# Optimization experiments

Measured on AMD Instinct MI355X. Metric: run time of the kernel, lower is better.

## Reference

```python
import jax, jax.numpy as jnp
import numpy as np

INF = 1e9
EPS = 1e-5

def layer_norm(x, g, b):
    mu = jnp.mean(x, axis=-1, keepdims=True)
    var = jnp.mean(jnp.square(x - mu), axis=-1, keepdims=True)
    return (x - mu) * jax.lax.rsqrt(var + EPS) * g + b

def setup_inputs() -> dict:
    key = jax.random.key(0)
    ks = jax.random.split(key, 12)
    B, S, N = 1, 512, 384
    c_in, c_hid, c_z, H = 64, 32, 128, 8
    d = c_hid * H
    sc = lambda fan: 1.0 / np.sqrt(fan)
    return {
        "m": jax.random.normal(ks[0], (B, S, N, c_in), jnp.float32),
        "z": jax.random.normal(ks[1], (B, N, N, c_z), jnp.float32),
        "mask": jnp.ones((B, N, N), jnp.float32),
        "gamma_m": jnp.ones((c_in,), jnp.float32),
        "beta_m": jnp.zeros((c_in,), jnp.float32),
        "gamma_z": jnp.ones((c_z,), jnp.float32),
        "beta_z": jnp.zeros((c_z,), jnp.float32),
        "w_z": jax.random.normal(ks[2], (c_z, H), jnp.float32) * sc(c_z),
        "b_z": jnp.zeros((H,), jnp.float32),
        "w_v": jax.random.normal(ks[3], (c_in, d), jnp.float32) * sc(c_in),
        "b_v": jnp.zeros((d,), jnp.float32),
        "w_g": jax.random.normal(ks[4], (c_in, d), jnp.float32) * sc(c_in),
        "b_g": jnp.zeros((d,), jnp.float32),
        "w_o": jax.random.normal(ks[5], (d, c_in), jnp.float32) * sc(d),
        "b_o": jnp.zeros((c_in,), jnp.float32),
    }

def reference(m, z, mask, gamma_m, beta_m, gamma_z, beta_z,
              w_z, b_z, w_v, b_v, w_g, b_g, w_o, b_o):
    B, S, N, c_in = m.shape
    H = w_z.shape[-1]
    C = w_v.shape[-1] // H
    # pair branch: LN -> linear -> [B,H,Nq,Nk] logits + mask bias -> softmax
    zn = layer_norm(z, gamma_z, beta_z)
    logits = jnp.einsum('bqkz,zh->bhqk', zn, w_z) + b_z[None, :, None, None]
    logits = logits + (INF * (mask - 1.0))[:, None, :, :]
    w = jax.nn.softmax(logits, axis=-1)                      # [B,H,Nq,Nk]
    # MSA branch: LN -> value / gate projections
    mn = layer_norm(m, gamma_m, beta_m)
    v = (mn @ w_v + b_v).reshape(B, S, N, H, C)              # [B,S,Nk,H,C]
    o = jnp.einsum('bhqk,bskhc->bsqhc', w, v)                # broadcast over S
    g = jax.nn.sigmoid(mn @ w_g + b_g).reshape(B, S, N, H, C)
    out = (o * g).reshape(B, S, N, H * C) @ w_o + b_o
    return out
```

## Files before the change

### kernel.cpp

```cpp
#include <hip/hip_runtime.h>
#include <hip/hip_bf16.h>

#define INFV 1e9f
#define EPSV 1e-5f

typedef unsigned short u16;
typedef unsigned int u32;
typedef __attribute__((ext_vector_type(8))) short short8;
typedef __attribute__((ext_vector_type(4))) float float4v;

__device__ __forceinline__ u16 f2us(float f) {
    u32 v;
    __builtin_memcpy(&v, &f, 4);
    u32 r = v + 0x7fffu + ((v >> 16) & 1u);
    return (u16)(r >> 16);
}

__device__ __forceinline__ float wred_sum(float x) {
    #pragma unroll
    for (int o = 32; o; o >>= 1) x += __shfl_xor(x, o);
    return x;
}
__device__ __forceinline__ float wred_max(float x) {
    #pragma unroll
    for (int o = 32; o; o >>= 1) x = fmaxf(x, __shfl_xor(x, o));
    return x;
}

__device__ __forceinline__ void gld16(const void* g, void* l) {
    __builtin_amdgcn_global_load_lds(
        (const __attribute__((address_space(1))) unsigned int*)g,
        (__attribute__((address_space(3))) unsigned int*)l,
        16, 0, 0);
}

__global__ __launch_bounds__(256) void k_prep_ln(
    const float* __restrict__ m, const float* __restrict__ gm, const float* __restrict__ bm,
    u16* __restrict__ mn,
    const float* __restrict__ wv, const float* __restrict__ wg,
    const float* __restrict__ wo, const float* __restrict__ wz,
    u16* __restrict__ wv_t, u16* __restrict__ wg_t,
    u16* __restrict__ wo_t, u16* __restrict__ wzT)
{
    if (blockIdx.x < 12288) {
        const int tid  = threadIdx.x;
        const int wid  = tid >> 6;
        const int lane = tid & 63;
        const int rloc = lane >> 4;
        const int c4   = (lane & 15) * 4;
        const int row  = blockIdx.x * 16 + wid * 4 + rloc;
        const float4 x = *(const float4*)(m + (size_t)row * 64 + c4);
        float s1 = x.x + x.y + x.z + x.w;
        float s2 = x.x * x.x + x.y * x.y + x.z * x.z + x.w * x.w;
        #pragma unroll
        for (int o = 8; o; o >>= 1) { s1 += __shfl_xor(s1, o); s2 += __shfl_xor(s2, o); }
        const float mean = s1 * (1.0f / 64.0f);
        const float var  = s2 * (1.0f / 64.0f) - mean * mean;
        const float rs   = rsqrtf(var + EPSV);
        const float4 g = *(const float4*)(gm + c4);
        const float4 b = *(const float4*)(bm + c4);
        uint2 pk;
        pk.x = (u32)f2us((x.x - mean) * rs * g.x + b.x) | ((u32)f2us((x.y - mean) * rs * g.y + b.y) << 16);
        pk.y = (u32)f2us((x.z - mean) * rs * g.z + b.z) | ((u32)f2us((x.w - mean) * rs * g.w + b.w) << 16);
        *(uint2*)(mn + (size_t)row * 64 + c4) = pk;
    } else {
        const int i = (blockIdx.x - 12288) * 256 + threadIdx.x;
        if (i < 16384) {
            const int n = i >> 6, k = i & 63;
            wv_t[i] = f2us(wv[(size_t)k * 256 + n]);
        } else if (i < 32768) {
            const int j = i - 16384, n = j >> 6, k = j & 63;
            wg_t[j] = f2us(wg[(size_t)k * 256 + n]);
        } else if (i < 49152) {
            const int j = i - 32768, n = j >> 8, k = j & 255;
            wo_t[j] = f2us(wo[(size_t)k * 64 + n]);
        } else if (i < 51200) {
            const int j = i - 49152, n = j >> 7, k = j & 127;
            wzT[j] = (n < 8) ? f2us(wz[(size_t)k * 8 + n]) : (u16)0;
        }
    }
}

__global__ __launch_bounds__(256) void k_vT(
    const u16* __restrict__ mn, const u16* __restrict__ wv_t, u16* __restrict__ vTf)
{
    const int tid  = threadIdx.x;
    const int wid  = tid >> 6;
    const int lane = tid & 63;
    const int lrow = lane & 15;
    const int lkg  = lane >> 4;
    const int s    = blockIdx.y;
    const int k0   = blockIdx.x * 64 + wid * 16;

    const int kt   = blockIdx.x * 2 + (wid >> 1);
    const int lkgc = (wid & 1) * 2 + (lkg >> 1);
    const int joff = (lkg & 1) * 4;

    const u16* mnk = mn + ((size_t)s * 384 + k0 + lrow) * 64;
    const short8 a0 = *(const short8*)(mnk + lkg * 8);
    const short8 a1 = *(const short8*)(mnk + 32 + lkg * 8);

    #pragma unroll
    for (int nt = 0; nt < 16; nt++) {
        const short8 b0 = *(const short8*)(wv_t + (size_t)(nt * 16 + lrow) * 64 + lkg * 8);
        const short8 b1 = *(const short8*)(wv_t + (size_t)(nt * 16 + lrow) * 64 + 32 + lkg * 8);
        float4v acc = (float4v){0.f, 0.f, 0.f, 0.f};
        acc = __builtin_amdgcn_mfma_f32_16x16x32_bf16(a0, b0, acc, 0, 0, 0);
        acc = __builtin_amdgcn_mfma_f32_16x16x32_bf16(a1, b1, acc, 0, 0, 0);
        uint2 pk;
        pk.x = (u32)f2us(acc[0]) | ((u32)f2us(acc[1]) << 16);
        pk.y = (u32)f2us(acc[2]) | ((u32)f2us(acc[3]) << 16);
        *(uint2*)(vTf + ((((size_t)s * 12 + kt) * 16 + nt) << 9)
                      + ((lkgc << 4) + lrow) * 8 + joff) = pk;
    }
}

__global__ __launch_bounds__(256) void k_logits2(
    const float* __restrict__ z, const float* __restrict__ mask,
    const float* __restrict__ gz, const float* __restrict__ bz,
    const u16* __restrict__ wzT, const float* __restrict__ bzb,
    float* __restrict__ wbuf)
{
    const int tid   = threadIdx.x;
    const int wid   = tid >> 6;
    const int lane  = tid & 63;
    const int lrow  = lane & 15;
    const int lkg   = lane >> 4;
    const int pair0 = (blockIdx.x * 4 + wid) * 16;

    float x[4][8];
    float s1 = 0.0f, s2 = 0.0f;
    #pragma unroll
    for (int ks = 0; ks < 4; ks++) {
        const float4* zp = (const float4*)(z + (size_t)(pair0 + lrow) * 128 + ks * 32 + lkg * 8);
        const float4 a = zp[0], b = zp[1];
        x[ks][0] = a.x; x[ks][1] = a.y; x[ks][2] = a.z; x[ks][3] = a.w;
        x[ks][4] = b.x; x[ks][5] = b.y; x[ks][6] = b.z; x[ks][7] = b.w;
        #pragma unroll
        for (int j = 0; j < 8; j++) { s1 += x[ks][j]; s2 += x[ks][j] * x[ks][j]; }
    }
    s1 += __shfl_xor(s1, 16); s1 += __shfl_xor(s1, 32);
    s2 += __shfl_xor(s2, 16); s2 += __shfl_xor(s2, 32);
    const float mean = s1 * (1.0f / 128.0f);
    const float var  = s2 * (1.0f / 128.0f) - mean * mean;
    const float rs   = rsqrtf(var + EPSV);

    float4v acc = (float4v){0.f, 0.f, 0.f, 0.f};
    #pragma unroll
    for (int ks = 0; ks < 4; ks++) {
        const int c0 = ks * 32 + lkg * 8;
        const float4 g0 = *(const float4*)(gz + c0);
        const float4 g1 = *(const float4*)(gz + c0 + 4);
        const float4 b0 = *(const float4*)(bz + c0);
        const float4 b1 = *(const float4*)(bz + c0 + 4);
        const float gv[8] = {g0.x, g0.y, g0.z, g0.w, g1.x, g1.y, g1.z, g1.w};
        const float bvv[8] = {b0.x, b0.y, b0.z, b0.w, b1.x, b1.y, b1.z, b1.w};
        short8 afr;
        #pragma unroll
        for (int j = 0; j < 8; j++)
            afr[j] = (short)f2us((x[ks][j] - mean) * rs * gv[j] + bvv[j]);
        const short8 bfr = *(const short8*)(wzT + (size_t)lrow * 128 + c0);
        acc = __builtin_amdgcn_mfma_f32_16x16x32_bf16(afr, bfr, acc, 0, 0, 0);
    }
    if (lrow < 8) {
        const float bzv = bzb[lrow];
        #pragma unroll
        for (int r = 0; r < 4; r++) {
            const int p = pair0 + lkg * 4 + r;
            const float mb = INFV * (mask[p] - 1.0f);
            wbuf[(size_t)lrow * 147456 + p] = acc[r] + bzv + mb;
        }
    }
}

__global__ __launch_bounds__(256) void k_softmax_f2(
    const float* __restrict__ wbuf, u16* __restrict__ wbf)
{
    __shared__ __align__(16) u16 lds[16 * 392];

    const int tid  = threadIdx.x;
    const int w    = tid >> 6;
    const int lane = tid & 63;
    const int rg   = lane >> 4;
    const int l16  = lane & 15;

    const int bx = blockIdx.x;
    const int h  = bx & 7;
    const int qm = bx >> 3;
    const int qb = qm >> 1;
    const int mt = qm & 1;
    const int rb = w * 4 + rg;
    const int q  = qb * 32 + mt * 16 + rb;

    const float* base = wbuf + (size_t)h * 147456 + (size_t)q * 384 + l16 * 24;
    float v[24];
    float mx = -1e30f;
    #pragma unroll
    for (int i = 0; i < 6; i++) {
        const float4 x = *(const float4*)(base + i * 4);
        v[i * 4 + 0] = x.x; v[i * 4 + 1] = x.y; v[i * 4 + 2] = x.z; v[i * 4 + 3] = x.w;
        mx = fmaxf(mx, fmaxf(fmaxf(x.x, x.y), fmaxf(x.z, x.w)));
    }
    #pragma unroll
    for (int o = 8; o; o >>= 1) mx = fmaxf(mx, __shfl_xor(mx, o));
    float s = 0.0f;
    #pragma unroll
    for (int i = 0; i < 24; i++) { v[i] = __expf(v[i] - mx); s += v[i]; }
    #pragma unroll
    for (int o = 8; o; o >>= 1) s += __shfl_xor(s, o);
    const float inv = 1.0f / s;

    u16* lp = lds + rb * 392 + l16 * 24;
    #pragma unroll
    for (int i = 0; i < 12; i++) {
        const u32 pk = (u32)f2us(v[2 * i] * inv) | ((u32)f2us(v[2 * i + 1] * inv) << 16);
        *(u32*)(lp + 2 * i) = pk;
    }
    __syncthreads();

    const int lr  = lane & 15;
    const int lkg = lane >> 4;
    #pragma unroll
    for (int j = 0; j < 3; j++) {
        const int kt = w * 3 + j;
        const short8 f = *(const short8*)(lds + lr * 392 + kt * 32 + lkg * 8);
        *(short8*)(wbf + ((((size_t)(qb * 8 + h) * 12 + kt) * 2 + mt) << 9) + lane * 8) = f;
    }
}

__global__ __launch_bounds__(256) void k_softmax(
    const float* __restrict__ wbuf, u16* __restrict__ wb16)
{
    const int r = blockIdx.x * 4 + (threadIdx.x >> 6);
    const int lane = threadIdx.x & 63;
    const float* base = wbuf + (size_t)r * 384;
    float v[6];
    float mx = -1e30f;
    #pragma unroll
    for (int j = 0; j < 6; j++) {
        v[j] = base[lane + j * 64];
        mx = fmaxf(mx, v[j]);
    }
    mx = wred_max(mx);
    float s = 0.0f;
    #pragma unroll
    for (int j = 0; j < 6; j++) {
        v[j] = __expf(v[j] - mx);
        s += v[j];
    }
    s = wred_sum(s);
    const float inv = 1.0f / s;
    u16* ob = wb16 + (size_t)r * 384;
    #pragma unroll
    for (int j = 0; j < 6; j++) ob[lane + j * 64] = f2us(v[j] * inv);
}

__global__ __launch_bounds__(512, 4) void k_fused9(
    const u16* __restrict__ mn, const u16* __restrict__ vTf,
    const float* __restrict__ bv, const float* __restrict__ bg, const float* __restrict__ bo,
    const u16* __restrict__ wg_t, const u16* __restrict__ wo_t,
    const u16* __restrict__ wbf, float* __restrict__ out)
{
    __shared__ __align__(16) char smem[67584];
    u16* vtt = (u16*)smem;
    u16* og  = (u16*)smem;

    const int tid  = threadIdx.x;
    const int w    = tid >> 6;
    const int wq   = w >> 1;
    const int wh   = w & 1;
    const int lane = tid & 63;
    const int lrow = lane & 15;
    const int lkg  = lane >> 4;
    const int stg  = w * 4;

    const int bid  = blockIdx.x;
    const int xcd  = bid & 7;
    const int slot = bid >> 3;
    const int sdiv = slot / 3;
    const int q0   = (slot - sdiv * 3) * 128;
    const int s    = sdiv * 8 + xcd;

    const int qb = (q0 >> 5) + wq;

    float4v oacc[16];
    #pragma unroll
    for (int mt = 0; mt < 2; mt++)
        #pragma unroll
        for (int nt = 0; nt < 8; nt++) {
            const float b = bv[wh * 128 + nt * 16 + lrow];
            oacc[mt * 8 + nt] = (float4v){b, b, b, b};
        }

    const u16* vfs = vTf + (((size_t)s * 12) << 13);

    {
        const u16* gp = vfs + ((size_t)stg << 9) + lane * 8;
        u16* lp = vtt + stg * 512;
        #pragma unroll
        for (int i = 0; i < 4; i++) gld16(gp + i * 512, lp + i * 512);
    }
    __syncthreads();

    for (int pt = 0; pt < 6; pt++) {
        const int cur = pt & 1;
        if (pt < 5) {
            const u16* gp = vfs + ((size_t)((pt + 1) * 32 + stg) << 9) + lane * 8;
            u16* lp = vtt + ((cur ^ 1) * 32 + stg) * 512;
            #pragma unroll
            for (int i = 0; i < 4; i++) gld16(gp + i * 512, lp + i * 512);
        }
        #pragma unroll 1
        for (int sub = 0; sub < 2; sub++) {
            const int kt = pt * 2 + sub;
            const u16* vb = vtt + (cur * 32 + sub * 16) * 512;
            #pragma unroll
            for (int hl = 0; hl < 4; hl++) {
                const size_t abase = (((size_t)(qb * 8 + wh * 4 + hl) * 12 + kt) * 2) << 9;
                const short8 a0 = *(const short8*)(wbf + abase + lane * 8);
                const short8 a1 = *(const short8*)(wbf + abase + 512 + lane * 8);
                const short8 b0 = *(const short8*)(vb + ((wh * 8 + hl * 2) * 512) + lane * 8);
                const short8 b1 = *(const short8*)(vb + ((wh * 8 + hl * 2 + 1) * 512) + lane * 8);
                const int nt = hl * 2;
                oacc[nt]         = __builtin_amdgcn_mfma_f32_16x16x32_bf16(a0, b0, oacc[nt], 0, 0, 0);
                oacc[8 + nt]     = __builtin_amdgcn_mfma_f32_16x16x32_bf16(a1, b0, oacc[8 + nt], 0, 0, 0);
                oacc[nt + 1]     = __builtin_amdgcn_mfma_f32_16x16x32_bf16(a0, b1, oacc[nt + 1], 0, 0, 0);
                oacc[8 + nt + 1] = __builtin_amdgcn_mfma_f32_16x16x32_bf16(a1, b1, oacc[8 + nt + 1], 0, 0, 0);
            }
        }
        __syncthreads();
    }

    {
        const u16* mnq = mn + ((size_t)s * 384 + q0 + wq * 32 + lrow) * 64;
        #pragma unroll
        for (int mt = 0; mt < 2; mt++) {
            const short8 a0 = *(const short8*)(mnq + mt * 1024 + lkg * 8);
            const short8 a1 = *(const short8*)(mnq + mt * 1024 + 32 + lkg * 8);
            #pragma unroll
            for (int nt = 0; nt < 8; nt++) {
                const int hc0 = wh * 128 + nt * 16;
                const float bgv = bg[hc0 + lrow];
                const short8 b0 = *(const short8*)(wg_t + (size_t)(hc0 + lrow) * 64 + lkg * 8);
                const short8 b1 = *(const short8*)(wg_t + (size_t)(hc0 + lrow) * 64 + 32 + lkg * 8);
                float4v gacc = (float4v){bgv, bgv, bgv, bgv};
                gacc = __builtin_amdgcn_mfma_f32_16x16x32_bf16(a0, b0, gacc, 0, 0, 0);
                gacc = __builtin_amdgcn_mfma_f32_16x16x32_bf16(a1, b1, gacc, 0, 0, 0);
                #pragma unroll
                for (int r = 0; r < 4; r++) {
                    const float sg = 1.0f / (1.0f + __expf(-gacc[r]));
                    og[(size_t)(wq * 32 + mt * 16 + lkg * 4 + r) * 264 + hc0 + lrow]
                        = f2us(oacc[mt * 8 + nt][r] * sg);
                }
            }
        }
    }
    __syncthreads();

    #pragma unroll
    for (int mt = 0; mt < 2; mt++) {
        short8 af[8];
        #pragma unroll
        for (int ks = 0; ks < 8; ks++)
            af[ks] = *(const short8*)&og[(size_t)(wq * 32 + mt * 16 + lrow) * 264 + ks * 32 + lkg * 8];
        #pragma unroll
        for (int ntl = 0; ntl < 2; ntl++) {
            const int nto = wh * 2 + ntl;
            const float bov = bo[nto * 16 + lrow];
            float4v fac = (float4v){bov, bov, bov, bov};
            #pragma unroll
            for (int ks = 0; ks < 8; ks++) {
                const short8 b = *(const short8*)(wo_t + (size_t)(nto * 16 + lrow) * 256 + ks * 32 + lkg * 8);
                fac = __builtin_amdgcn_mfma_f32_16x16x32_bf16(af[ks], b, fac, 0, 0, 0);
            }
            #pragma unroll
            for (int r = 0; r < 4; r++)
                out[((size_t)s * 384 + q0 + wq * 32 + mt * 16 + lkg * 4 + r) * 64 + nto * 16 + lrow]
                    = fac[r];
        }
    }
}

__global__ __launch_bounds__(256, 2) void k_fused4(
    const u16* __restrict__ mn,
    const float* __restrict__ bv, const float* __restrict__ bg, const float* __restrict__ bo,
    const u16* __restrict__ wv_t, const u16* __restrict__ wg_t, const u16* __restrict__ wo_t,
    const u16* __restrict__ wb16, float* __restrict__ out)
{
    __shared__ __align__(16) char smem[67584];
    u16* vtt = (u16*)smem;
    u16* og  = (u16*)smem;

    const int tid  = threadIdx.x;
    const int wid  = tid >> 6;
    const int lane = tid & 63;
    const int lrow = lane & 15;
    const int lkg  = lane >> 4;
    const int s    = blockIdx.y;
    const int q0   = blockIdx.x * 128;

    const int vmt  = wid & 1;
    const int vnt0 = (wid >> 1) * 8;

    float4v oacc[32];
    #pragma unroll
    for (int mt = 0; mt < 2; mt++)
        #pragma unroll
        for (int nt = 0; nt < 16; nt++) {
            const float b = bv[nt * 16 + lrow];
            oacc[mt * 16 + nt] = (float4v){b, b, b, b};
        }

    for (int kt = 0; kt < 12; kt++) {
        const int k0 = kt * 32;
        float4v vacc[8];
        #pragma unroll
        for (int nt = 0; nt < 8; nt++) vacc[nt] = (float4v){0.f, 0.f, 0.f, 0.f};
        const u16* mnk = mn + ((size_t)s * 384 + k0 + vmt * 16 + lrow) * 64;
        #pragma unroll
        for (int ks = 0; ks < 2; ks++) {
            const short8 a = *(const short8*)(mnk + ks * 32 + lkg * 8);
            #pragma unroll
            for (int nt = 0; nt < 8; nt++) {
                const short8 b = *(const short8*)(wv_t + (size_t)((vnt0 + nt) * 16 + lrow) * 64 + ks * 32 + lkg * 8);
                vacc[nt] = __builtin_amdgcn_mfma_f32_16x16x32_bf16(a, b, vacc[nt], 0, 0, 0);
            }
        }
        u16* vb = vtt + (size_t)(kt & 1) * 8192;
        const int kg8 = vmt * 2 + (lkg >> 1);
        const int ko  = (lkg & 1) * 4;
        #pragma unroll
        for (int nt = 0; nt < 8; nt++) {
            uint2 pk;
            pk.x = (u32)f2us(vacc[nt][0]) | ((u32)f2us(vacc[nt][1]) << 16);
            pk.y = (u32)f2us(vacc[nt][2]) | ((u32)f2us(vacc[nt][3]) << 16);
            *(uint2*)&vb[((size_t)kg8 * 256 + (vnt0 + nt) * 16 + lrow) * 8 + ko] = pk;
        }
        __syncthreads();

        short8 ah[2][8];
        #pragma unroll
        for (int mt = 0; mt < 2; mt++)
            #pragma unroll
            for (int h = 0; h < 8; h++)
                ah[mt][h] = *(const short8*)(wb16 + (size_t)h * 147456
                              + (size_t)(q0 + wid * 32 + mt * 16 + lrow) * 384 + k0 + lkg * 8);
        #pragma unroll
        for (int nt = 0; nt < 16; nt++) {
            const short8 b = *(const short8*)&vb[((size_t)lkg * 256 + nt * 16 + lrow) * 8];
            oacc[nt]      = __builtin_amdgcn_mfma_f32_16x16x32_bf16(ah[0][nt >> 1], b, oacc[nt], 0, 0, 0);
            oacc[16 + nt] = __builtin_amdgcn_mfma_f32_16x16x32_bf16(ah[1][nt >> 1], b, oacc[16 + nt], 0, 0, 0);
        }
    }
    __syncthreads();

    #pragma unroll
    for (int mt = 0; mt < 2; mt++) {
        const u16* mnq = mn + ((size_t)s * 384 + q0 + wid * 32 + mt * 16 + lrow) * 64;
        const short8 a0 = *(const short8*)(mnq + lkg * 8);
        const short8 a1 = *(const short8*)(mnq + 32 + lkg * 8);
        #pragma unroll
        for (int nt = 0; nt < 16; nt++) {
            const float bgv = bg[nt * 16 + lrow];
            float4v gacc = (float4v){bgv, bgv, bgv, bgv};
            const short8 b0 = *(const short8*)(wg_t + (size_t)(nt * 16 + lrow) * 64 + lkg * 8);
            const short8 b1 = *(const short8*)(wg_t + (size_t)(nt * 16 + lrow) * 64 + 32 + lkg * 8);
            gacc = __builtin_amdgcn_mfma_f32_16x16x32_bf16(a0, b0, gacc, 0, 0, 0);
            gacc = __builtin_amdgcn_mfma_f32_16x16x32_bf16(a1, b1, gacc, 0, 0, 0);
            #pragma unroll
            for (int r = 0; r < 4; r++) {
                const float sg = 1.0f / (1.0f + __expf(-gacc[r]));
                og[(size_t)(wid * 32 + mt * 16 + lkg * 4 + r) * 264 + nt * 16 + lrow]
                    = f2us(oacc[mt * 16 + nt][r] * sg);
            }
        }
    }
    __syncthreads();

    #pragma unroll
    for (int mt = 0; mt < 2; mt++) {
        short8 af[8];
        #pragma unroll
        for (int ks = 0; ks < 8; ks++)
            af[ks] = *(const short8*)&og[(size_t)(wid * 32 + mt * 16 + lrow) * 264 + ks * 32 + lkg * 8];
        #pragma unroll
        for (int nt = 0; nt < 4; nt++) {
            const float bov = bo[nt * 16 + lrow];
            float4v fac = (float4v){bov, bov, bov, bov};
            #pragma unroll
            for (int ks = 0; ks < 8; ks++) {
                const short8 b = *(const short8*)(wo_t + (size_t)(nt * 16 + lrow) * 256 + ks * 32 + lkg * 8);
                fac = __builtin_amdgcn_mfma_f32_16x16x32_bf16(af[ks], b, fac, 0, 0, 0);
            }
            #pragma unroll
            for (int r = 0; r < 4; r++)
                out[((size_t)s * 384 + q0 + wid * 32 + mt * 16 + lkg * 4 + r) * 64 + nt * 16 + lrow]
                    = fac[r];
        }
    }
}

extern "C" void kernel_launch(void* const* d_in, const int* in_sizes, int n_in,
                              void* d_out, int out_size, void* d_ws, size_t ws_size,
                              hipStream_t stream) {
    const float* m    = (const float*)d_in[0];
    const float* z    = (const float*)d_in[1];
    const float* mask = (const float*)d_in[2];
    const float* gm   = (const float*)d_in[3];
    const float* bm   = (const float*)d_in[4];
    const float* gz   = (const float*)d_in[5];
    const float* bz   = (const float*)d_in[6];
    const float* wz   = (const float*)d_in[7];
    const float* bzb  = (const float*)d_in[8];
    const float* wv   = (const float*)d_in[9];
    const float* bv   = (const float*)d_in[10];
    const float* wg   = (const float*)d_in[11];
    const float* bg   = (const float*)d_in[12];
    const float* wo   = (const float*)d_in[13];
    const float* bo   = (const float*)d_in[14];
    float* out = (float*)d_out;

    char* ws = (char*)d_ws;
    float* wbuf = (float*)ws;
    u16*  wb16  = (u16*)(ws + 4718592);
    u16*  mn    = (u16*)(ws + 7077888);
    u16*  wv_t  = (u16*)(ws + 32243712);
    u16*  wg_t  = (u16*)(ws + 32276480);
    u16*  wo_t  = (u16*)(ws + 32309248);
    u16*  wzT   = (u16*)(ws + 32342016);
    u16*  vTf   = (u16*)(ws + 32346112);

    const bool big = ws_size >= 133009408ull;

    k_prep_ln<<<12488, 256, 0, stream>>>(m, gm, bm, mn, wv, wg, wo, wz, wv_t, wg_t, wo_t, wzT);
    if (big)
        k_vT<<<dim3(6, 512), 256, 0, stream>>>(mn, wv_t, vTf);
    k_logits2<<<2304, 256, 0, stream>>>(z, mask, gz, bz, wzT, bzb, wbuf);
    if (big) {
        k_softmax_f2<<<192, 256, 0, stream>>>(wbuf, wb16);
        k_fused9<<<1536, 512, 0, stream>>>(mn, vTf, bv, bg, bo, wg_t, wo_t, wb16, out);
    } else {
        k_softmax<<<768, 256, 0, stream>>>(wbuf, wb16);
        k_fused4<<<dim3(3, 512), 256, 0, stream>>>(mn, bv, bg, bo, wv_t, wg_t, wo_t, wb16, out);
    }
}
```

Measured before the change: 386.9 us.

## Process two MSA rows per block to reuse attention weight fragments

The fused attention/gate/output kernel now runs 1024-thread blocks that each cover two sequence rows (s0, s0+1) for a 128-query tile. Each wave loads its softmax-weight A fragments once per k-tile and applies them to the V tiles of both rows, which halves global reads of the weight matrix. The wave-to-head split is re-partitioned so each wave owns 4 head-column tiles, and LDS doubles to about 132KB. The larger LDS footprint and block size cut occupancy to one block per CU, which may limit latency hiding.

```diff
diff --git a/kernel.cpp b/kernel.cpp
--- a/kernel.cpp
+++ b/kernel.cpp
@@ -255,91 +255,97 @@
     for (int j = 0; j < 6; j++) ob[lane + j * 64] = f2us(v[j] * inv);
 }
 
-__global__ __launch_bounds__(512, 4) void k_fused9(
+__global__ __launch_bounds__(1024, 4) void k_fused11(
     const u16* __restrict__ mn, const u16* __restrict__ vTf,
     const float* __restrict__ bv, const float* __restrict__ bg, const float* __restrict__ bo,
     const u16* __restrict__ wg_t, const u16* __restrict__ wo_t,
     const u16* __restrict__ wbf, float* __restrict__ out)
 {
-    __shared__ __align__(16) char smem[67584];
+    __shared__ __align__(16) char smem[135168];
     u16* vtt = (u16*)smem;
     u16* og  = (u16*)smem;
 
     const int tid  = threadIdx.x;
     const int w    = tid >> 6;
-    const int wq   = w >> 1;
-    const int wh   = w & 1;
+    const int wq   = w & 3;
+    const int wh   = (w >> 2) & 3;
     const int lane = tid & 63;
     const int lrow = lane & 15;
     const int lkg  = lane >> 4;
-    const int stg  = w * 4;
 
     const int bid  = blockIdx.x;
     const int xcd  = bid & 7;
     const int slot = bid >> 3;
-    const int sdiv = slot / 3;
-    const int q0   = (slot - sdiv * 3) * 128;
-    const int s    = sdiv * 8 + xcd;
+    const int spd  = slot / 3;
+    const int qi   = slot - spd * 3;
+    const int q0   = qi * 128;
+    const int sp   = spd * 8 + xcd;
+    const int s0   = sp * 2;
 
     const int qb = (q0 >> 5) + wq;
 
     float4v oacc[16];
     #pragma unroll
-    for (int mt = 0; mt < 2; mt++)
-        #pragma unroll
-        for (int nt = 0; nt < 8; nt++) {
-            const float b = bv[wh * 128 + nt * 16 + lrow];
-            oacc[mt * 8 + nt] = (float4v){b, b, b, b};
-        }
-
-    const u16* vfs = vTf + (((size_t)s * 12) << 13);
+    for (int ntl = 0; ntl < 4; ntl++) {
+        const float b = bv[(wh * 4 + ntl) * 16 + lrow];
+        #pragma unroll
+        for (int sm = 0; sm < 4; sm++) oacc[sm * 4 + ntl] = (float4v){b, b, b, b};
+    }
+
+    const u16* wAb0 = wbf + (((size_t)(qb * 8 + wh * 2 + 0) * 24) << 9);
+    const u16* wAb1 = wbf + (((size_t)(qb * 8 + wh * 2 + 1) * 24) << 9);
+
+    const int ssg  = (w * 2) >> 4;
+    const int nt0  = (w * 2) & 15;
+    const u16* vstg = vTf + ((((size_t)(s0 + ssg) * 12) * 16 + nt0) << 9) + lane * 8;
 
     {
-        const u16* gp = vfs + ((size_t)stg << 9) + lane * 8;
-        u16* lp = vtt + stg * 512;
-        #pragma unroll
-        for (int i = 0; i < 4; i++) gld16(gp + i * 512, lp + i * 512);
+        u16* lp = vtt + (ssg * 16 + nt0) * 512;
+        gld16(vstg, lp);
+        gld16(vstg + 512, lp + 512);
     }
     __syncthreads();
 
-    for (int pt = 0; pt < 6; pt++) {
-        const int cur = pt & 1;
-        if (pt < 5) {
-            const u16* gp = vfs + ((size_t)((pt + 1) * 32 + stg) << 9) + lane * 8;
-            u16* lp = vtt + ((cur ^ 1) * 32 + stg) * 512;
-            #pragma unroll
-            for (int i = 0; i < 4; i++) gld16(gp + i * 512, lp + i * 512);
-        }
-        #pragma unroll 1
-        for (int sub = 0; sub < 2; sub++) {
-            const int kt = pt * 2 + sub;
-            const u16* vb = vtt + (cur * 32 + sub * 16) * 512;
-            #pragma unroll
-            for (int hl = 0; hl < 4; hl++) {
-                const size_t abase = (((size_t)(qb * 8 + wh * 4 + hl) * 12 + kt) * 2) << 9;
-                const short8 a0 = *(const short8*)(wbf + abase + lane * 8);
-                const short8 a1 = *(const short8*)(wbf + abase + 512 + lane * 8);
-                const short8 b0 = *(const short8*)(vb + ((wh * 8 + hl * 2) * 512) + lane * 8);
-                const short8 b1 = *(const short8*)(vb + ((wh * 8 + hl * 2 + 1) * 512) + lane * 8);
-                const int nt = hl * 2;
-                oacc[nt]         = __builtin_amdgcn_mfma_f32_16x16x32_bf16(a0, b0, oacc[nt], 0, 0, 0);
-                oacc[8 + nt]     = __builtin_amdgcn_mfma_f32_16x16x32_bf16(a1, b0, oacc[8 + nt], 0, 0, 0);
-                oacc[nt + 1]     = __builtin_amdgcn_mfma_f32_16x16x32_bf16(a0, b1, oacc[nt + 1], 0, 0, 0);
-                oacc[8 + nt + 1] = __builtin_amdgcn_mfma_f32_16x16x32_bf16(a1, b1, oacc[8 + nt + 1], 0, 0, 0);
+    for (int kt = 0; kt < 12; kt++) {
+        const int cur = kt & 1;
+        if (kt < 11) {
+            const u16* gp = vstg + (((size_t)(kt + 1) * 16) << 9);
+            u16* lp = vtt + (((cur ^ 1) * 2 + ssg) * 16 + nt0) * 512;
+            gld16(gp, lp);
+            gld16(gp + 512, lp + 512);
+        }
+        const size_t aoff = (size_t)kt << 10;
+        const short8 a00 = *(const short8*)(wAb0 + aoff + lane * 8);
+        const short8 a01 = *(const short8*)(wAb0 + aoff + 512 + lane * 8);
+        const short8 a10 = *(const short8*)(wAb1 + aoff + lane * 8);
+        const short8 a11 = *(const short8*)(wAb1 + aoff + 512 + lane * 8);
+        #pragma unroll
+        for (int ss = 0; ss < 2; ss++) {
+            const u16* vb = vtt + ((cur * 2 + ss) * 16 + wh * 4) * 512;
+            #pragma unroll
+            for (int ntl = 0; ntl < 4; ntl++) {
+                const short8 b = *(const short8*)(vb + ntl * 512 + lane * 8);
+                const short8 am0 = (ntl < 2) ? a00 : a10;
+                const short8 am1 = (ntl < 2) ? a01 : a11;
+                oacc[ss * 8 + ntl]     = __builtin_amdgcn_mfma_f32_16x16x32_bf16(am0, b, oacc[ss * 8 + ntl], 0, 0, 0);
+                oacc[ss * 8 + 4 + ntl] = __builtin_amdgcn_mfma_f32_16x16x32_bf16(am1, b, oacc[ss * 8 + 4 + ntl], 0, 0, 0);
             }
         }
         __syncthreads();
     }
 
-    {
+    #pragma unroll
+    for (int ss = 0; ss < 2; ss++) {
+        const int s = s0 + ss;
         const u16* mnq = mn + ((size_t)s * 384 + q0 + wq * 32 + lrow) * 64;
+        u16* ogs = og + ss * 33792;
         #pragma unroll
         for (int mt = 0; mt < 2; mt++) {
             const short8 a0 = *(const short8*)(mnq + mt * 1024 + lkg * 8);
             const short8 a1 = *(const short8*)(mnq + mt * 1024 + 32 + lkg * 8);
             #pragma unroll
-            for (int nt = 0; nt < 8; nt++) {
-                const int hc0 = wh * 128 + nt * 16;
+            for (int ntl = 0; ntl < 4; ntl++) {
+                const int hc0 = (wh * 4 + ntl) * 16;
                 const float bgv = bg[hc0 + lrow];
                 const short8 b0 = *(const short8*)(wg_t + (size_t)(hc0 + lrow) * 64 + lkg * 8);
                 const short8 b1 = *(const short8*)(wg_t + (size_t)(hc0 + lrow) * 64 + 32 + lkg * 8);
@@ -349,34 +355,42 @@
                 #pragma unroll
                 for (int r = 0; r < 4; r++) {
                     const float sg = 1.0f / (1.0f + __expf(-gacc[r]));
-                    og[(size_t)(wq * 32 + mt * 16 + lkg * 4 + r) * 264 + hc0 + lrow]
-                        = f2us(oacc[mt * 8 + nt][r] * sg);
+                    ogs[(size_t)(wq * 32 + mt * 16 + lkg * 4 + r) * 264 + hc0 + lrow]
+                        = f2us(oacc[ss * 8 + mt * 4 + ntl][r] * sg);
                 }
             }
         }
     }
     __syncthreads();
 
-    #pragma unroll
-    for (int mt = 0; mt < 2; mt++) {
-        short8 af[8];
-        #pragma unroll
-        for (int ks = 0; ks < 8; ks++)
-            af[ks] = *(const short8*)&og[(size_t)(wq * 32 + mt * 16 + lrow) * 264 + ks * 32 + lkg * 8];
-        #pragma unroll
-        for (int ntl = 0; ntl < 2; ntl++) {
-            const int nto = wh * 2 + ntl;
-            const float bov = bo[nto * 16 + lrow];
-            float4v fac = (float4v){bov, bov, bov, bov};
-            #pragma unroll
-            for (int ks = 0; ks < 8; ks++) {
-                const short8 b = *(const short8*)(wo_t + (size_t)(nto * 16 + lrow) * 256 + ks * 32 + lkg * 8);
-                fac = __builtin_amdgcn_mfma_f32_16x16x32_bf16(af[ks], b, fac, 0, 0, 0);
+    {
+        const int ws  = w >> 3;
+        const int w8  = w & 7;
+        const int wq8 = w8 >> 1;
+        const int wh8 = w8 & 1;
+        const int s   = s0 + ws;
+        const u16* ogs = og + ws * 33792;
+        #pragma unroll
+        for (int mt = 0; mt < 2; mt++) {
+            short8 af[8];
+            #pragma unroll
+            for (int ks = 0; ks < 8; ks++)
+                af[ks] = *(const short8*)(ogs + (size_t)(wq8 * 32 + mt * 16 + lrow) * 264 + ks * 32 + lkg * 8);
+            #pragma unroll
+            for (int ntl = 0; ntl < 2; ntl++) {
+                const int nto = wh8 * 2 + ntl;
+                const float bov = bo[nto * 16 + lrow];
+                float4v fac = (float4v){bov, bov, bov, bov};
+                #pragma unroll
+                for (int ks = 0; ks < 8; ks++) {
+                    const short8 b = *(const short8*)(wo_t + (size_t)(nto * 16 + lrow) * 256 + ks * 32 + lkg * 8);
+                    fac = __builtin_amdgcn_mfma_f32_16x16x32_bf16(af[ks], b, fac, 0, 0, 0);
+                }
+                #pragma unroll
+                for (int r = 0; r < 4; r++)
+                    out[((size_t)s * 384 + q0 + wq8 * 32 + mt * 16 + lkg * 4 + r) * 64 + nto * 16 + lrow]
+                        = fac[r];
             }
-            #pragma unroll
-            for (int r = 0; r < 4; r++)
-                out[((size_t)s * 384 + q0 + wq * 32 + mt * 16 + lkg * 4 + r) * 64 + nto * 16 + lrow]
-                    = fac[r];
         }
     }
 }
@@ -538,7 +552,7 @@
     k_logits2<<<2304, 256, 0, stream>>>(z, mask, gz, bz, wzT, bzb, wbuf);
     if (big) {
         k_softmax_f2<<<192, 256, 0, stream>>>(wbuf, wb16);
-        k_fused9<<<1536, 512, 0, stream>>>(mn, vTf, bv, bg, bo, wg_t, wo_t, wb16, out);
+        k_fused11<<<768, 1024, 0, stream>>>(mn, vTf, bv, bg, bo, wg_t, wo_t, wb16, out);
     } else {
         k_softmax<<<768, 256, 0, stream>>>(wbuf, wb16);
         k_fused4<<<dim3(3, 512), 256, 0, stream>>>(mn, bv, bg, bo, wv_t, wg_t, wo_t, wb16, out);
```

New measurement: 397.1 us. 2.6% more time.
